# Optimization experiments

Hardware: AMD Instinct MI355X
Metric: run time of the kernel (lower is better)

Reference implementation:

```python
import jax, jax.numpy as jnp
import numpy as np

N, S, Q, P = 100000, 64, 50, 3  # pauli words, heads, qubits, pauli basis
EPS = 1e-12  # F.normalize clamp


def setup_inputs() -> dict:
    key = jax.random.key(0)
    k1, k2, k3, k4 = jax.random.split(key, 4)
    return {
        "batch_pauli_tensor": jax.random.uniform(k1, (N, Q, P), dtype=jnp.float32),
        "batch_coeff": jax.random.normal(k2, (N,), dtype=jnp.float32),
        "heads_param": jax.random.normal(k3, (S, Q, P), dtype=jnp.float32),
        "head_ratios_param": jax.random.normal(k4, (S,), dtype=jnp.float32),
    }


def reference(batch_pauli_tensor, batch_coeff, heads_param, head_ratios_param):
    s = heads_param.shape[0]
    heads = jax.nn.softplus(heads_param * 20.0)
    heads = heads / jnp.maximum(jnp.sum(heads, axis=-1, keepdims=True), EPS)
    hr = jax.nn.softplus(head_ratios_param * 20.0)
    hr = hr / jnp.maximum(jnp.sum(hr), EPS)
    hr = (hr + 0.001 / s) / 1.001
    # coverage: per-(word, head, qubit) match prob -> product over qubits -> ratio-weighted sum
    cov = jnp.einsum('nqp,sqp->nsq', batch_pauli_tensor, heads)  # [n, s, q]
    cov = jnp.prod(cov, axis=-1)                                 # [n, s]
    cov = jnp.einsum('s,ns->n', hr, cov)                         # [n]
    # variance loss
    return jnp.sum(batch_coeff ** 2 / cov)
```

## Files before the change

kernel.cpp:

```cpp
#include <hip/hip_runtime.h>
#include <math.h>

#define N_Q 50
#define N_P 3
#define N_S 64
#define ROW 150
#define BLK_ROWS 256
#define THREADS 256
#define WAVES 4
#define SCHUNK 16
#define RPL 4

#define WS_CNT_OFF 3200
#define WS_HP_OFF 3264
#define WS_HRV_OFF 41664

__device__ __forceinline__ float softplus20(float x) {
    float z = x * 20.0f;
    return fmaxf(z, 0.0f) + log1pf(expf(-fabsf(z)));
}

__global__ void precompute_kernel(const float* __restrict__ heads_param,
                                  const float* __restrict__ hr_param,
                                  float* __restrict__ HP,
                                  float* __restrict__ hrv,
                                  int* __restrict__ cnt) {
    const int tid = threadIdx.x;
    if (blockIdx.x == 0) {
        if (tid == 0) *cnt = 0;
        if (tid < N_S) {
            float sp = softplus20(hr_param[tid]);
            float tot = sp;
            #pragma unroll
            for (int off = 32; off; off >>= 1) tot += __shfl_xor(tot, off);
            float hr = sp / fmaxf(tot, 1e-12f);
            hrv[tid] = (hr + 0.001f / (float)N_S) / 1.001f;
        }
    }
    int idx = blockIdx.x * blockDim.x + tid;
    if (idx < N_S * N_Q) {
        int q = idx / N_S;
        int s = idx - q * N_S;
        const float* hp = heads_param + ((size_t)s * N_Q + q) * N_P;
        float sp0 = softplus20(hp[0]);
        float sp1 = softplus20(hp[1]);
        float sp2 = softplus20(hp[2]);
        float denom = fmaxf(sp0 + sp1 + sp2, 1e-12f);
        float* o = HP + ((size_t)q * N_S + s) * 3;
        o[0] = sp0 / denom;
        o[1] = sp1 / denom;
        o[2] = sp2 / denom;
    }
}

__device__ __forceinline__ void computeQ4(const float4* __restrict__ Hq,
                                          const float (&a)[RPL][3],
                                          float (&p)[RPL][SCHUNK]) {
    #pragma unroll
    for (int g = 0; g < 4; ++g) {
        float4 b0 = Hq[3 * g], b1 = Hq[3 * g + 1], b2 = Hq[3 * g + 2];
        #pragma unroll
        for (int r = 0; r < RPL; ++r) {
            p[r][4*g+0] *= fmaf(b0.x, a[r][0], fmaf(b0.y, a[r][1], b0.z * a[r][2]));
            p[r][4*g+1] *= fmaf(b0.w, a[r][0], fmaf(b1.x, a[r][1], b1.y * a[r][2]));
            p[r][4*g+2] *= fmaf(b1.z, a[r][0], fmaf(b1.w, a[r][1], b2.x * a[r][2]));
            p[r][4*g+3] *= fmaf(b2.y, a[r][0], fmaf(b2.z, a[r][1], b2.w * a[r][2]));
        }
    }
}

__global__ __launch_bounds__(THREADS, 2) void main_kernel(
    const float* __restrict__ A, const float* __restrict__ coeff,
    const float* __restrict__ HP, const float* __restrict__ hrv,
    double* __restrict__ partials, int* __restrict__ cnt,
    float* __restrict__ out, int N) {
    __shared__ float hHs[N_Q * N_S * 3];
    __shared__ float hrvl[N_S];
    __shared__ float covs[WAVES][BLK_ROWS];
    __shared__ double redd[WAVES];
    __shared__ double redf[WAVES];
    __shared__ int isLast;

    const int tid = threadIdx.x;
    const int lane = tid & 63;
    const int wave = tid >> 6;
    const int nbase = blockIdx.x * BLK_ROWS;

    for (int i = tid; i < (N_Q * N_S * 3) / 4; i += THREADS)
        ((float4*)hHs)[i] = ((const float4*)HP)[i];
    if (tid < N_S) hrvl[tid] = hrv[tid];
    __syncthreads();

    const float2* __restrict__ pR[RPL];
    #pragma unroll
    for (int r = 0; r < RPL; ++r) {
        int n = nbase + 64 * r + lane;  if (n >= N) n = N - 1;
        pR[r] = (const float2*)A + (size_t)n * (ROW / 2);
    }

    float prod[RPL][SCHUNK];
    #pragma unroll
    for (int r = 0; r < RPL; ++r)
        #pragma unroll
        for (int i = 0; i < SCHUNK; ++i) prod[r][i] = 1.0f;

    const float4* __restrict__ Hbase = (const float4*)hHs + 12 * wave;

    float2 x[RPL][3];
    #pragma unroll
    for (int r = 0; r < RPL; ++r) {
        x[r][0] = pR[r][0]; x[r][1] = pR[r][1]; x[r][2] = pR[r][2];
    }

    #pragma unroll 5
    for (int w = 0; w < N_Q / 2; ++w) {
        const int nb = (w < N_Q / 2 - 1) ? 3 * w + 3 : 0;
        float2 nx[RPL][3];
        #pragma unroll
        for (int r = 0; r < RPL; ++r) {
            nx[r][0] = pR[r][nb]; nx[r][1] = pR[r][nb + 1]; nx[r][2] = pR[r][nb + 2];
        }
        const float4* Hq = Hbase + 96 * w;
        float aq[RPL][3], cq[RPL][3];
        #pragma unroll
        for (int r = 0; r < RPL; ++r) {
            aq[r][0] = x[r][0].x; aq[r][1] = x[r][0].y; aq[r][2] = x[r][1].x;
            cq[r][0] = x[r][1].y; cq[r][1] = x[r][2].x; cq[r][2] = x[r][2].y;
        }
        computeQ4(Hq,      aq, prod);
        computeQ4(Hq + 48, cq, prod);
        #pragma unroll
        for (int r = 0; r < RPL; ++r) {
            x[r][0] = nx[r][0]; x[r][1] = nx[r][1]; x[r][2] = nx[r][2];
        }
    }

    const int s0 = wave * SCHUNK;
    #pragma unroll
    for (int r = 0; r < RPL; ++r) {
        float acc = 0.0f;
        #pragma unroll
        for (int i = 0; i < SCHUNK; ++i) acc = fmaf(hrvl[s0 + i], prod[r][i], acc);
        covs[wave][64 * r + lane] = acc;
    }
    __syncthreads();

    {
        const int row = 64 * wave + lane;
        const int n = nbase + row;
        float cov = covs[0][row] + covs[1][row] + covs[2][row] + covs[3][row];
        float term = 0.0f;
        if (n < N) { float c = coeff[n]; term = (c * c) / cov; }
        double td = (double)term;
        #pragma unroll
        for (int off = 32; off; off >>= 1) td += __shfl_down(td, off);
        if (lane == 0) redd[wave] = td;
    }
    __syncthreads();

    if (tid == 0) {
        partials[blockIdx.x] = ((redd[0] + redd[1]) + redd[2]) + redd[3];
        __threadfence();
        int v = atomicAdd(cnt, 1);
        isLast = (v == (int)gridDim.x - 1);
    }
    __syncthreads();

    if (isLast) {
        __threadfence();
        double s = 0.0;
        for (int i = tid; i < (int)gridDim.x; i += THREADS) s += partials[i];
        #pragma unroll
        for (int off = 32; off; off >>= 1) s += __shfl_down(s, off);
        if (lane == 0) redf[wave] = s;
        __syncthreads();
        if (tid == 0) {
            double t = 0.0;
            #pragma unroll
            for (int wv = 0; wv < WAVES; ++wv) t += redf[wv];
            out[0] = (float)t;
        }
    }
}

extern "C" void kernel_launch(void* const* d_in, const int* in_sizes, int n_in,
                              void* d_out, int out_size, void* d_ws, size_t ws_size,
                              hipStream_t stream) {
    const float* A           = (const float*)d_in[0];
    const float* coeff       = (const float*)d_in[1];
    const float* heads_param = (const float*)d_in[2];
    const float* hr_param    = (const float*)d_in[3];
    const int N = in_sizes[1];
    const int nblocks = (N + BLK_ROWS - 1) / BLK_ROWS;

    char* ws = (char*)d_ws;
    double* partials = (double*)ws;
    int*   cnt = (int*)(ws + WS_CNT_OFF);
    float* HP  = (float*)(ws + WS_HP_OFF);
    float* hrv = (float*)(ws + WS_HRV_OFF);
    float* out = (float*)d_out;

    const int pre_blocks = (N_S * N_Q + THREADS - 1) / THREADS;
    precompute_kernel<<<pre_blocks, THREADS, 0, stream>>>(heads_param, hr_param,
                                                          HP, hrv, cnt);
    main_kernel<<<nblocks, THREADS, 0, stream>>>(A, coeff, HP, hrv, partials,
                                                 cnt, out, N);
}
```

Measured before the change: 152.5 us.

## Transpose pauli tensor to column-major float2 layout before main kernel

Adds a transpose kernel that rewrites the input tensor into a [75][N] float2 layout in workspace. The main kernel then reads it with coalesced per-lane loads instead of strided 600-byte-row loads. This adds a full extra read and write pass over the 60MB input and an extra launch. If the workspace is too small, the code falls back to the original kernel.

After: 177.3 us. 1.16x slower.

```diff
diff --git a/kernel.cpp b/kernel.cpp
--- a/kernel.cpp
+++ b/kernel.cpp
@@ -14,6 +14,7 @@
 #define WS_CNT_OFF 3200
 #define WS_HP_OFF 3264
 #define WS_HRV_OFF 41664
+#define WS_AT_OFF 65536
 
 __device__ __forceinline__ float softplus20(float x) {
     float z = x * 20.0f;
@@ -53,6 +54,33 @@
     }
 }
 
+__global__ __launch_bounds__(THREADS) void transpose_kernel(
+    const float* __restrict__ A, float2* __restrict__ AT2, int N) {
+    __shared__ float tile[64 * 151];
+    const int tid = threadIdx.x;
+    const int nbase = blockIdx.x * 64;
+    const float2* __restrict__ Asrc = (const float2*)A;
+    for (int g = tid; g < 64 * (ROW / 2); g += THREADS) {
+        int r = g / (ROW / 2);
+        int j = g - r * (ROW / 2);
+        int src = nbase + r; if (src >= N) src = N - 1;
+        float2 v = Asrc[(size_t)src * (ROW / 2) + j];
+        tile[r * 151 + 2 * j]     = v.x;
+        tile[r * 151 + 2 * j + 1] = v.y;
+    }
+    __syncthreads();
+    for (int g = tid; g < (ROW / 2) * 64; g += THREADS) {
+        int j2 = g >> 6;
+        int nloc = g & 63;
+        int n = nbase + nloc;
+        if (n < N) {
+            float2 v = make_float2(tile[nloc * 151 + 2 * j2],
+                                   tile[nloc * 151 + 2 * j2 + 1]);
+            AT2[(size_t)j2 * N + n] = v;
+        }
+    }
+}
+
 __device__ __forceinline__ void computeQ4(const float4* __restrict__ Hq,
                                           const float (&a)[RPL][3],
                                           float (&p)[RPL][SCHUNK]) {
@@ -69,7 +97,133 @@
     }
 }
 
-__global__ __launch_bounds__(THREADS, 2) void main_kernel(
+__device__ __forceinline__ void epilogue(
+    float (*covs)[BLK_ROWS], const float* __restrict__ coeff,
+    double* __restrict__ partials, int* __restrict__ cnt,
+    float* __restrict__ out, int N, int nbase,
+    int tid, int lane, int wave, double* redd, double* redf, int* isLast) {
+    {
+        const int row = 64 * wave + lane;
+        const int n = nbase + row;
+        float cov = covs[0][row] + covs[1][row] + covs[2][row] + covs[3][row];
+        float term = 0.0f;
+        if (n < N) { float c = coeff[n]; term = (c * c) / cov; }
+        double td = (double)term;
+        #pragma unroll
+        for (int off = 32; off; off >>= 1) td += __shfl_down(td, off);
+        if (lane == 0) redd[wave] = td;
+    }
+    __syncthreads();
+
+    if (tid == 0) {
+        partials[blockIdx.x] = ((redd[0] + redd[1]) + redd[2]) + redd[3];
+        __threadfence();
+        int v = atomicAdd(cnt, 1);
+        *isLast = (v == (int)gridDim.x - 1);
+    }
+    __syncthreads();
+
+    if (*isLast) {
+        __threadfence();
+        double s = 0.0;
+        for (int i = tid; i < (int)gridDim.x; i += THREADS) s += partials[i];
+        #pragma unroll
+        for (int off = 32; off; off >>= 1) s += __shfl_down(s, off);
+        if (lane == 0) redf[wave] = s;
+        __syncthreads();
+        if (tid == 0) {
+            double t = 0.0;
+            #pragma unroll
+            for (int wv = 0; wv < WAVES; ++wv) t += redf[wv];
+            out[0] = (float)t;
+        }
+    }
+}
+
+__global__ __launch_bounds__(THREADS, 2) void main_kernel_t(
+    const float2* __restrict__ AT2, const float* __restrict__ coeff,
+    const float* __restrict__ HP, const float* __restrict__ hrv,
+    double* __restrict__ partials, int* __restrict__ cnt,
+    float* __restrict__ out, int N) {
+    __shared__ float hHs[N_Q * N_S * 3];
+    __shared__ float hrvl[N_S];
+    __shared__ float covs[WAVES][BLK_ROWS];
+    __shared__ double redd[WAVES];
+    __shared__ double redf[WAVES];
+    __shared__ int isLast;
+
+    const int tid = threadIdx.x;
+    const int lane = tid & 63;
+    const int wave = tid >> 6;
+    const int nbase = blockIdx.x * BLK_ROWS;
+
+    for (int i = tid; i < (N_Q * N_S * 3) / 4; i += THREADS)
+        ((float4*)hHs)[i] = ((const float4*)HP)[i];
+    if (tid < N_S) hrvl[tid] = hrv[tid];
+    __syncthreads();
+
+    const float2* __restrict__ Qp[RPL];
+    #pragma unroll
+    for (int r = 0; r < RPL; ++r) {
+        int n = nbase + 64 * r + lane;  if (n >= N) n = N - 1;
+        Qp[r] = AT2 + n;
+    }
+    const size_t Ns = (size_t)N;
+
+    float prod[RPL][SCHUNK];
+    #pragma unroll
+    for (int r = 0; r < RPL; ++r)
+        #pragma unroll
+        for (int i = 0; i < SCHUNK; ++i) prod[r][i] = 1.0f;
+
+    const float4* __restrict__ Hbase = (const float4*)hHs + 12 * wave;
+
+    float2 x[RPL][3];
+    #pragma unroll
+    for (int r = 0; r < RPL; ++r) {
+        x[r][0] = Qp[r][0]; x[r][1] = Qp[r][Ns]; x[r][2] = Qp[r][2 * Ns];
+    }
+
+    size_t o = 0;
+    #pragma unroll 5
+    for (int w = 0; w < N_Q / 2; ++w) {
+        const size_t on = (w < N_Q / 2 - 1) ? o + 3 * Ns : (size_t)0;
+        float2 nx[RPL][3];
+        #pragma unroll
+        for (int r = 0; r < RPL; ++r) {
+            nx[r][0] = Qp[r][on]; nx[r][1] = Qp[r][on + Ns]; nx[r][2] = Qp[r][on + 2 * Ns];
+        }
+        const float4* Hq = Hbase + 96 * w;
+        float aq[RPL][3], cq[RPL][3];
+        #pragma unroll
+        for (int r = 0; r < RPL; ++r) {
+            aq[r][0] = x[r][0].x; aq[r][1] = x[r][0].y; aq[r][2] = x[r][1].x;
+            cq[r][0] = x[r][1].y; cq[r][1] = x[r][2].x; cq[r][2] = x[r][2].y;
+        }
+        computeQ4(Hq,      aq, prod);
+        computeQ4(Hq + 48, cq, prod);
+        #pragma unroll
+        for (int r = 0; r < RPL; ++r) {
+            x[r][0] = nx[r][0]; x[r][1] = nx[r][1]; x[r][2] = nx[r][2];
+        }
+        o = on;
+    }
+
+    const int s0 = wave * SCHUNK;
+    #pragma unroll
+    for (int r = 0; r < RPL; ++r) {
+        float acc = 0.0f;
+        #pragma unroll
+        for (int i = 0; i < SCHUNK; ++i) acc = fmaf(hrvl[s0 + i], prod[r][i], acc);
+        covs[wave][64 * r + lane] = acc;
+    }
+    __syncthreads();
+
+    epilogue(covs, coeff, partials, cnt, out, N, nbase, tid, lane, wave,
+             redd, redf, &isLast);
+}
+
+__global__ __launch_bounds__(THREADS, 2) void main_kernel_f(
     const float* __restrict__ A, const float* __restrict__ coeff,
     const float* __restrict__ HP, const float* __restrict__ hrv,
     double* __restrict__ partials, int* __restrict__ cnt,
@@ -145,42 +299,8 @@
     }
     __syncthreads();
 
-    {
-        const int row = 64 * wave + lane;
-        const int n = nbase + row;
-        float cov = covs[0][row] + covs[1][row] + covs[2][row] + covs[3][row];
-        float term = 0.0f;
-        if (n < N) { float c = coeff[n]; term = (c * c) / cov; }
-        double td = (double)term;
-        #pragma unroll
-        for (int off = 32; off; off >>= 1) td += __shfl_down(td, off);
-        if (lane == 0) redd[wave] = td;
-    }
-    __syncthreads();
-
-    if (tid == 0) {
-        partials[blockIdx.x] = ((redd[0] + redd[1]) + redd[2]) + redd[3];
-        __threadfence();
-        int v = atomicAdd(cnt, 1);
-        isLast = (v == (int)gridDim.x - 1);
-    }
-    __syncthreads();
-
-    if (isLast) {
-        __threadfence();
-        double s = 0.0;
-        for (int i = tid; i < (int)gridDim.x; i += THREADS) s += partials[i];
-        #pragma unroll
-        for (int off = 32; off; off >>= 1) s += __shfl_down(s, off);
-        if (lane == 0) redf[wave] = s;
-        __syncthreads();
-        if (tid == 0) {
-            double t = 0.0;
-            #pragma unroll
-            for (int wv = 0; wv < WAVES; ++wv) t += redf[wv];
-            out[0] = (float)t;
-        }
-    }
+    epilogue(covs, coeff, partials, cnt, out, N, nbase, tid, lane, wave,
+             redd, redf, &isLast);
 }
 
 extern "C" void kernel_launch(void* const* d_in, const int* in_sizes, int n_in,
@@ -195,14 +315,24 @@
 
     char* ws = (char*)d_ws;
     double* partials = (double*)ws;
-    int*   cnt = (int*)(ws + WS_CNT_OFF);
-    float* HP  = (float*)(ws + WS_HP_OFF);
-    float* hrv = (float*)(ws + WS_HRV_OFF);
-    float* out = (float*)d_out;
+    int*    cnt = (int*)(ws + WS_CNT_OFF);
+    float*  HP  = (float*)(ws + WS_HP_OFF);
+    float*  hrv = (float*)(ws + WS_HRV_OFF);
+    float2* AT2 = (float2*)(ws + WS_AT_OFF);
+    float*  out = (float*)d_out;
 
     const int pre_blocks = (N_S * N_Q + THREADS - 1) / THREADS;
     precompute_kernel<<<pre_blocks, THREADS, 0, stream>>>(heads_param, hr_param,
                                                           HP, hrv, cnt);
-    main_kernel<<<nblocks, THREADS, 0, stream>>>(A, coeff, HP, hrv, partials,
-                                                 cnt, out, N);
-}
+
+    const size_t at_bytes = (size_t)(ROW / 2) * (size_t)N * sizeof(float2);
+    if (ws_size >= (size_t)WS_AT_OFF + at_bytes) {
+        const int tblocks = (N + 63) / 64;
+        transpose_kernel<<<tblocks, THREADS, 0, stream>>>(A, AT2, N);
+        main_kernel_t<<<nblocks, THREADS, 0, stream>>>(AT2, coeff, HP, hrv,
+                                                       partials, cnt, out, N);
+    } else {
+        main_kernel_f<<<nblocks, THREADS, 0, stream>>>(A, coeff, HP, hrv,
+                                                       partials, cnt, out, N);
+    }
+}
```

## Fuse precompute into single persistent-grid kernel with split LDS/global row paths

Applied to the files above, without the earlier changes.

Removes the separate precompute kernel: each block recomputes the softplus-normalized heads and head ratios directly into shared memory, and the counter is reset with a memset. The grid is fixed at 256 blocks of 512 threads, each covering about 391 rows. Within a block, 128 rows are staged in a padded LDS tile and handled by four waves, while the other four waves stream the remaining rows from global memory with register prefetch. This cuts launch overhead and matches the grid to the CU count, at the cost of redundant per-block head preprocessing, more LDS use, and possibly uneven work between the two wave groups.

Result: slower. 174.6 us (+14.5%).

```diff
diff --git a/kernel.cpp b/kernel.cpp
--- a/kernel.cpp
+++ b/kernel.cpp
@@ -5,161 +5,198 @@
 #define N_P 3
 #define N_S 64
 #define ROW 150
-#define BLK_ROWS 256
-#define THREADS 256
-#define WAVES 4
+#define THREADS 512
+#define GRID 256
 #define SCHUNK 16
-#define RPL 4
+#define L_ROWS 128
+#define S_SLOTS 5
+#define SLOTS 448
+#define ASTRIDE 151
+#define NF2 75
 
 #define WS_CNT_OFF 3200
-#define WS_HP_OFF 3264
-#define WS_HRV_OFF 41664
 
 __device__ __forceinline__ float softplus20(float x) {
     float z = x * 20.0f;
     return fmaxf(z, 0.0f) + log1pf(expf(-fabsf(z)));
 }
 
-__global__ void precompute_kernel(const float* __restrict__ heads_param,
-                                  const float* __restrict__ hr_param,
-                                  float* __restrict__ HP,
-                                  float* __restrict__ hrv,
-                                  int* __restrict__ cnt) {
+template <int R>
+__device__ __forceinline__ void computeQR(const float4* __restrict__ Hq,
+                                          const float (&a)[R][3],
+                                          float (&p)[R][SCHUNK]) {
+    #pragma unroll
+    for (int g = 0; g < 4; ++g) {
+        float4 b0 = Hq[3 * g], b1 = Hq[3 * g + 1], b2 = Hq[3 * g + 2];
+        #pragma unroll
+        for (int r = 0; r < R; ++r) {
+            p[r][4*g+0] *= fmaf(b0.x, a[r][0], fmaf(b0.y, a[r][1], b0.z * a[r][2]));
+            p[r][4*g+1] *= fmaf(b0.w, a[r][0], fmaf(b1.x, a[r][1], b1.y * a[r][2]));
+            p[r][4*g+2] *= fmaf(b1.z, a[r][0], fmaf(b1.w, a[r][1], b2.x * a[r][2]));
+            p[r][4*g+3] *= fmaf(b2.y, a[r][0], fmaf(b2.z, a[r][1], b2.w * a[r][2]));
+        }
+    }
+}
+
+__global__ __launch_bounds__(THREADS, 2) void main_kernel(
+    const float* __restrict__ A, const float* __restrict__ coeff,
+    const float* __restrict__ heads_param, const float* __restrict__ hr_param,
+    double* __restrict__ partials, int* __restrict__ cnt,
+    float* __restrict__ out, int N) {
+    __shared__ float hHs[N_Q * N_S * 3];
+    __shared__ float Atile[L_ROWS * ASTRIDE];
+    __shared__ float hrvl[N_S];
+    __shared__ float covs[4][SLOTS];
+    __shared__ double redd[8];
+    __shared__ double redf[8];
+    __shared__ int isLast;
+
     const int tid = threadIdx.x;
-    if (blockIdx.x == 0) {
-        if (tid == 0) *cnt = 0;
-        if (tid < N_S) {
-            float sp = softplus20(hr_param[tid]);
-            float tot = sp;
-            #pragma unroll
-            for (int off = 32; off; off >>= 1) tot += __shfl_xor(tot, off);
-            float hr = sp / fmaxf(tot, 1e-12f);
-            hrv[tid] = (hr + 0.001f / (float)N_S) / 1.001f;
-        }
-    }
-    int idx = blockIdx.x * blockDim.x + tid;
-    if (idx < N_S * N_Q) {
-        int q = idx / N_S;
-        int s = idx - q * N_S;
+    const int lane = tid & 63;
+    const int wave = tid >> 6;
+    const int b = blockIdx.x;
+
+    const int q0 = N / GRID, r0 = N % GRID;
+    const int base = b * q0 + (b < r0 ? b : r0);
+    const int count = q0 + (b < r0 ? 1 : 0);
+    const int cmax = (count > 0 ? count : 1) - 1;
+
+    if (tid < N_S) {
+        float sp = softplus20(hr_param[tid]);
+        float tot = sp;
+        #pragma unroll
+        for (int off = 32; off; off >>= 1) tot += __shfl_xor(tot, off);
+        float hr = sp / fmaxf(tot, 1e-12f);
+        hrvl[tid] = (hr + 0.001f / (float)N_S) / 1.001f;
+    }
+    for (int e = tid; e < N_S * N_Q; e += THREADS) {
+        int q = e / N_S;
+        int s = e - q * N_S;
         const float* hp = heads_param + ((size_t)s * N_Q + q) * N_P;
         float sp0 = softplus20(hp[0]);
         float sp1 = softplus20(hp[1]);
         float sp2 = softplus20(hp[2]);
         float denom = fmaxf(sp0 + sp1 + sp2, 1e-12f);
-        float* o = HP + ((size_t)q * N_S + s) * 3;
+        float* o = hHs + (q * N_S + s) * 3;
         o[0] = sp0 / denom;
         o[1] = sp1 / denom;
         o[2] = sp2 / denom;
     }
-}
-
-__device__ __forceinline__ void computeQ4(const float4* __restrict__ Hq,
-                                          const float (&a)[RPL][3],
-                                          float (&p)[RPL][SCHUNK]) {
+    {
+        const float2* __restrict__ Ag = (const float2*)A;
+        const size_t gb = (size_t)base * NF2;
+        for (int g = tid; g < L_ROWS * NF2; g += THREADS) {
+            int rr = g / NF2, c = g - rr * NF2;
+            int src = rr <= cmax ? rr : cmax;
+            float2 v = Ag[gb + (size_t)src * NF2 + c];
+            float* d = Atile + rr * ASTRIDE + 2 * c;
+            d[0] = v.x; d[1] = v.y;
+        }
+    }
+    __syncthreads();
+
+    const int sgrp = (wave < 4) ? wave : (wave - 4);
+    const float4* __restrict__ Hbase = (const float4*)hHs + 12 * sgrp;
+    const int s0 = sgrp * SCHUNK;
+
+    if (wave < 4) {
+        const float2* __restrict__ pS[S_SLOTS];
+        #pragma unroll
+        for (int j = 0; j < S_SLOTS; ++j) {
+            int slot = L_ROWS + 64 * j + lane;
+            int rr = slot <= cmax ? slot : cmax;
+            pS[j] = (const float2*)A + ((size_t)base + rr) * NF2;
+        }
+        float prod[S_SLOTS][SCHUNK];
+        #pragma unroll
+        for (int j = 0; j < S_SLOTS; ++j)
+            #pragma unroll
+            for (int i = 0; i < SCHUNK; ++i) prod[j][i] = 1.0f;
+
+        float2 x[S_SLOTS][3];
+        #pragma unroll
+        for (int j = 0; j < S_SLOTS; ++j) {
+            x[j][0] = pS[j][0]; x[j][1] = pS[j][1]; x[j][2] = pS[j][2];
+        }
+        #pragma unroll 5
+        for (int w = 0; w < N_Q / 2; ++w) {
+            const int nb = (w < N_Q / 2 - 1) ? 3 * w + 3 : 0;
+            float2 nx[S_SLOTS][3];
+            #pragma unroll
+            for (int j = 0; j < S_SLOTS; ++j) {
+                nx[j][0] = pS[j][nb]; nx[j][1] = pS[j][nb + 1]; nx[j][2] = pS[j][nb + 2];
+            }
+            const float4* Hq = Hbase + 96 * w;
+            float aq[S_SLOTS][3], cq[S_SLOTS][3];
+            #pragma unroll
+            for (int j = 0; j < S_SLOTS; ++j) {
+                aq[j][0] = x[j][0].x; aq[j][1] = x[j][0].y; aq[j][2] = x[j][1].x;
+                cq[j][0] = x[j][1].y; cq[j][1] = x[j][2].x; cq[j][2] = x[j][2].y;
+            }
+            computeQR<S_SLOTS>(Hq,      aq, prod);
+            computeQR<S_SLOTS>(Hq + 48, cq, prod);
+            #pragma unroll
+            for (int j = 0; j < S_SLOTS; ++j) {
+                x[j][0] = nx[j][0]; x[j][1] = nx[j][1]; x[j][2] = nx[j][2];
+            }
+        }
+        #pragma unroll
+        for (int j = 0; j < S_SLOTS; ++j) {
+            float acc = 0.0f;
+            #pragma unroll
+            for (int i = 0; i < SCHUNK; ++i) acc = fmaf(hrvl[s0 + i], prod[j][i], acc);
+            covs[sgrp][L_ROWS + 64 * j + lane] = acc;
+        }
+    } else {
+        const float* __restrict__ Ar0 = Atile + lane * ASTRIDE;
+        const float* __restrict__ Ar1 = Atile + (lane + 64) * ASTRIDE;
+        float prod[2][SCHUNK];
+        #pragma unroll
+        for (int j = 0; j < 2; ++j)
+            #pragma unroll
+            for (int i = 0; i < SCHUNK; ++i) prod[j][i] = 1.0f;
+
+        #pragma unroll 5
+        for (int w = 0; w < N_Q / 2; ++w) {
+            const int o = 6 * w;
+            float aq[2][3] = {{Ar0[o], Ar0[o+1], Ar0[o+2]},
+                              {Ar1[o], Ar1[o+1], Ar1[o+2]}};
+            float cq[2][3] = {{Ar0[o+3], Ar0[o+4], Ar0[o+5]},
+                              {Ar1[o+3], Ar1[o+4], Ar1[o+5]}};
+            const float4* Hq = Hbase + 96 * w;
+            computeQR<2>(Hq,      aq, prod);
+            computeQR<2>(Hq + 48, cq, prod);
+        }
+        float acc0 = 0.0f, acc1 = 0.0f;
+        #pragma unroll
+        for (int i = 0; i < SCHUNK; ++i) {
+            acc0 = fmaf(hrvl[s0 + i], prod[0][i], acc0);
+            acc1 = fmaf(hrvl[s0 + i], prod[1][i], acc1);
+        }
+        covs[sgrp][lane]      = acc0;
+        covs[sgrp][64 + lane] = acc1;
+    }
+    __syncthreads();
+
+    double td = 0.0;
+    if (tid < SLOTS) {
+        const int slot = tid;
+        float cov = covs[0][slot] + covs[1][slot] + covs[2][slot] + covs[3][slot];
+        if (slot < count) {
+            float c = coeff[base + slot];
+            td = (double)((c * c) / cov);
+        }
+    }
     #pragma unroll
-    for (int g = 0; g < 4; ++g) {
-        float4 b0 = Hq[3 * g], b1 = Hq[3 * g + 1], b2 = Hq[3 * g + 2];
-        #pragma unroll
-        for (int r = 0; r < RPL; ++r) {
-            p[r][4*g+0] *= fmaf(b0.x, a[r][0], fmaf(b0.y, a[r][1], b0.z * a[r][2]));
-            p[r][4*g+1] *= fmaf(b0.w, a[r][0], fmaf(b1.x, a[r][1], b1.y * a[r][2]));
-            p[r][4*g+2] *= fmaf(b1.z, a[r][0], fmaf(b1.w, a[r][1], b2.x * a[r][2]));
-            p[r][4*g+3] *= fmaf(b2.y, a[r][0], fmaf(b2.z, a[r][1], b2.w * a[r][2]));
-        }
-    }
-}
-
-__global__ __launch_bounds__(THREADS, 2) void main_kernel(
-    const float* __restrict__ A, const float* __restrict__ coeff,
-    const float* __restrict__ HP, const float* __restrict__ hrv,
-    double* __restrict__ partials, int* __restrict__ cnt,
-    float* __restrict__ out, int N) {
-    __shared__ float hHs[N_Q * N_S * 3];
-    __shared__ float hrvl[N_S];
-    __shared__ float covs[WAVES][BLK_ROWS];
-    __shared__ double redd[WAVES];
-    __shared__ double redf[WAVES];
-    __shared__ int isLast;
-
-    const int tid = threadIdx.x;
-    const int lane = tid & 63;
-    const int wave = tid >> 6;
-    const int nbase = blockIdx.x * BLK_ROWS;
-
-    for (int i = tid; i < (N_Q * N_S * 3) / 4; i += THREADS)
-        ((float4*)hHs)[i] = ((const float4*)HP)[i];
-    if (tid < N_S) hrvl[tid] = hrv[tid];
-    __syncthreads();
-
-    const float2* __restrict__ pR[RPL];
-    #pragma unroll
-    for (int r = 0; r < RPL; ++r) {
-        int n = nbase + 64 * r + lane;  if (n >= N) n = N - 1;
-        pR[r] = (const float2*)A + (size_t)n * (ROW / 2);
-    }
-
-    float prod[RPL][SCHUNK];
-    #pragma unroll
-    for (int r = 0; r < RPL; ++r)
-        #pragma unroll
-        for (int i = 0; i < SCHUNK; ++i) prod[r][i] = 1.0f;
-
-    const float4* __restrict__ Hbase = (const float4*)hHs + 12 * wave;
-
-    float2 x[RPL][3];
-    #pragma unroll
-    for (int r = 0; r < RPL; ++r) {
-        x[r][0] = pR[r][0]; x[r][1] = pR[r][1]; x[r][2] = pR[r][2];
-    }
-
-    #pragma unroll 5
-    for (int w = 0; w < N_Q / 2; ++w) {
-        const int nb = (w < N_Q / 2 - 1) ? 3 * w + 3 : 0;
-        float2 nx[RPL][3];
-        #pragma unroll
-        for (int r = 0; r < RPL; ++r) {
-            nx[r][0] = pR[r][nb]; nx[r][1] = pR[r][nb + 1]; nx[r][2] = pR[r][nb + 2];
-        }
-        const float4* Hq = Hbase + 96 * w;
-        float aq[RPL][3], cq[RPL][3];
-        #pragma unroll
-        for (int r = 0; r < RPL; ++r) {
-            aq[r][0] = x[r][0].x; aq[r][1] = x[r][0].y; aq[r][2] = x[r][1].x;
-            cq[r][0] = x[r][1].y; cq[r][1] = x[r][2].x; cq[r][2] = x[r][2].y;
-        }
-        computeQ4(Hq,      aq, prod);
-        computeQ4(Hq + 48, cq, prod);
-        #pragma unroll
-        for (int r = 0; r < RPL; ++r) {
-            x[r][0] = nx[r][0]; x[r][1] = nx[r][1]; x[r][2] = nx[r][2];
-        }
-    }
-
-    const int s0 = wave * SCHUNK;
-    #pragma unroll
-    for (int r = 0; r < RPL; ++r) {
-        float acc = 0.0f;
-        #pragma unroll
-        for (int i = 0; i < SCHUNK; ++i) acc = fmaf(hrvl[s0 + i], prod[r][i], acc);
-        covs[wave][64 * r + lane] = acc;
-    }
-    __syncthreads();
-
-    {
-        const int row = 64 * wave + lane;
-        const int n = nbase + row;
-        float cov = covs[0][row] + covs[1][row] + covs[2][row] + covs[3][row];
-        float term = 0.0f;
-        if (n < N) { float c = coeff[n]; term = (c * c) / cov; }
-        double td = (double)term;
-        #pragma unroll
-        for (int off = 32; off; off >>= 1) td += __shfl_down(td, off);
-        if (lane == 0) redd[wave] = td;
-    }
+    for (int off = 32; off; off >>= 1) td += __shfl_down(td, off);
+    if (lane == 0) redd[wave] = td;
     __syncthreads();
 
     if (tid == 0) {
-        partials[blockIdx.x] = ((redd[0] + redd[1]) + redd[2]) + redd[3];
+        double bs = 0.0;
+        #pragma unroll
+        for (int wv = 0; wv < 8; ++wv) bs += redd[wv];
+        partials[b] = bs;
         __threadfence();
         int v = atomicAdd(cnt, 1);
         isLast = (v == (int)gridDim.x - 1);
@@ -177,7 +214,7 @@
         if (tid == 0) {
             double t = 0.0;
             #pragma unroll
-            for (int wv = 0; wv < WAVES; ++wv) t += redf[wv];
+            for (int wv = 0; wv < 8; ++wv) t += redf[wv];
             out[0] = (float)t;
         }
     }
@@ -191,18 +228,13 @@
     const float* heads_param = (const float*)d_in[2];
     const float* hr_param    = (const float*)d_in[3];
     const int N = in_sizes[1];
-    const int nblocks = (N + BLK_ROWS - 1) / BLK_ROWS;
 
     char* ws = (char*)d_ws;
     double* partials = (double*)ws;
     int*   cnt = (int*)(ws + WS_CNT_OFF);
-    float* HP  = (float*)(ws + WS_HP_OFF);
-    float* hrv = (float*)(ws + WS_HRV_OFF);
     float* out = (float*)d_out;
 
-    const int pre_blocks = (N_S * N_Q + THREADS - 1) / THREADS;
-    precompute_kernel<<<pre_blocks, THREADS, 0, stream>>>(heads_param, hr_param,
-                                                          HP, hrv, cnt);
-    main_kernel<<<nblocks, THREADS, 0, stream>>>(A, coeff, HP, hrv, partials,
-                                                 cnt, out, N);
-}
+    hipMemsetAsync(cnt, 0, sizeof(int), stream);
+    main_kernel<<<GRID, THREADS, 0, stream>>>(A, coeff, heads_param, hr_param,
+                                              partials, cnt, out, N);
+}
```
